# Optimization experiments

Hardware: AMD Instinct MI355X
Metric: run time of the kernel (lower is better)

## Reference

```python
import jax, jax.numpy as jnp
import numpy as np
from jax import lax

H, W = 128, 128
K_JUNC = 300
STEPS = 32
THRESH = 0.008
BIAS_SPAN = 1
SCALE = 5.0
SENTINEL = K_JUNC * K_JUNC


def decode_hafm(angs, dist, bias):
    # angs [B,3,H,W], dist [B,1,H,W], bias [B,1,H,W] -> lines [B,3,H,W,4]
    bias_range = jnp.arange(-BIAS_SPAN, BIAS_SPAN + 1, dtype=jnp.float32).reshape(1, -1, 1, 1)
    d = jnp.clip(dist + bias * bias_range, 0.0, 1.0)  # [B,3,H,W]
    angle0 = (angs[:, 0:1] - 0.5) * jnp.pi * 2
    angle1 = angs[:, 1:2] * jnp.pi / 2
    angle2 = -angs[:, 2:3] * jnp.pi / 2
    c0, s0 = jnp.cos(angle0), jnp.sin(angle0)
    t1, t2 = jnp.tan(angle1), jnp.tan(angle2)
    x1 = (c0 - s0 * t1) * d * SCALE
    y1 = (s0 + c0 * t1) * d * SCALE
    x2 = (c0 - s0 * t2) * d * SCALE
    y2 = (s0 + c0 * t2) * d * SCALE
    y0, x0 = jnp.meshgrid(jnp.arange(H, dtype=jnp.float32), jnp.arange(W, dtype=jnp.float32), indexing='ij')
    x0 = x0[None, None]
    y0 = y0[None, None]
    x1 = jnp.clip(x1 + x0, 0, W - 1)
    y1 = jnp.clip(y1 + y0, 0, H - 1)
    x2 = jnp.clip(x2 + x0, 0, W - 1)
    y2 = jnp.clip(y2 + y0, 0, H - 1)
    return jnp.stack((x1, y1, x2, y2), axis=-1)


def propose_junctions(jloc, joff):
    # jloc [H,W], joff [2,H,W]; 3x3 NMS + top-K, thresholded junctions
    pooled = lax.reduce_window(jloc, -jnp.inf, lax.max, (3, 3), (1, 1), 'SAME')
    nms = jnp.where(jloc == pooled, jloc, 0.0)
    scores, idx = lax.top_k(nms.reshape(-1), K_JUNC)
    y = (idx // W).astype(jnp.float32)
    x = (idx % W).astype(jnp.float32)
    xs = x + joff[0].reshape(-1)[idx]
    ys = y + joff[1].reshape(-1)[idx]
    coords = jnp.stack([xs, ys], axis=-1)  # [K,2]
    valid = scores > THRESH
    coords = jnp.where(valid[:, None], coords, 1e6)
    return coords, scores


def bilinear_sample(fmap, px, py):
    # fmap [C,H,W]; px,py [N,S] -> [C,N,S]
    C = fmap.shape[0]
    px = jnp.clip(px, 0.0, W - 1)
    py = jnp.clip(py, 0.0, H - 1)
    x0 = jnp.floor(px)
    y0 = jnp.floor(py)
    x0i = x0.astype(jnp.int32)
    y0i = y0.astype(jnp.int32)
    x1i = jnp.minimum(x0i + 1, W - 1)
    y1i = jnp.minimum(y0i + 1, H - 1)
    wx = px - x0
    wy = py - y0
    flat = fmap.reshape(C, H * W)

    def g(yi, xi):
        return flat[:, (yi * W + xi).reshape(-1)].reshape(C, *px.shape)

    return (g(y0i, x0i) * (1 - wx) * (1 - wy)
            + g(y0i, x1i) * wx * (1 - wy)
            + g(y1i, x0i) * (1 - wx) * wy
            + g(y1i, x1i) * wx * wy)


def setup_inputs() -> dict:
    key = jax.random.key(0)
    ks = jax.random.split(key, 10)
    return {
        'features': jax.random.normal(ks[0], (1, 256, H, W), jnp.float32),
        'heatmaps': jax.random.normal(ks[1], (1, 9, H, W), jnp.float32),
        'fc1_w': jax.random.normal(ks[2], (128, 256), jnp.float32) * 0.05,
        'fc1_b': jax.random.normal(ks[3], (128,), jnp.float32) * 0.05,
        'w1': jax.random.normal(ks[4], (1024, 1024), jnp.float32) * 0.03,
        'b1': jnp.zeros((1024,), jnp.float32),
        'w2': jax.random.normal(ks[5], (1024, 1024), jnp.float32) * 0.03,
        'b2': jnp.zeros((1024,), jnp.float32),
        'w3': jax.random.normal(ks[6], (1, 1024), jnp.float32) * 0.03,
        'b3': jnp.zeros((1,), jnp.float32),
    }


def reference(features, heatmaps, fc1_w, fc1_b, w1, b1, w2, b2, w3, b3):
    angs = jax.nn.sigmoid(heatmaps[:, 0:3])
    dist = jax.nn.sigmoid(heatmaps[:, 3:4])
    bias = jax.nn.sigmoid(heatmaps[:, 4:5])
    jloc = jax.nn.softmax(heatmaps[:, 5:7], axis=1)[0, 1]  # [H,W]
    joff = jax.nn.sigmoid(heatmaps[0, 7:9])                # [2,H,W]

    junc, _ = propose_junctions(jloc, joff)                # [K,2]
    lines = decode_hafm(angs, dist, bias).reshape(-1, 4)   # [N,4], N=3*H*W
    N = lines.shape[0]

    # junction-to-endpoint matching (cdist + argmin)
    d1 = ((junc[:, None, :] - lines[None, :, :2]) ** 2).sum(-1)  # [K,N]
    d2 = ((junc[:, None, :] - lines[None, :, 2:]) ** 2).sum(-1)
    j1 = jnp.argmin(d1, axis=0)
    j2 = jnp.argmin(d2, axis=0)
    lo = jnp.minimum(j1, j2)
    hi = jnp.maximum(j1, j2)
    ids = jnp.where(lo < hi, lo * K_JUNC + hi, SENTINEL)
    # fixed-size dedup (masked analogue of torch unique(dim=0))
    uids = jnp.unique(ids, size=N, fill_value=SENTINEL)
    valid = uids < SENTINEL
    uids_safe = jnp.where(valid, uids, 0)
    p1 = junc[uids_safe // K_JUNC]
    p2 = junc[uids_safe % K_JUNC]
    line_coords = jnp.where(valid[:, None], jnp.concatenate([p1, p2], axis=-1), 0.0)  # [N,4]

    # LOI feature sampling
    loi = jnp.einsum('oc,chw->ohw', fc1_w, features[0]) + fc1_b[:, None, None]  # [128,H,W]
    t = jnp.linspace(0.0, 1.0, STEPS)[None, :]
    px = line_coords[:, 0:1] * t + line_coords[:, 2:3] * (1 - t)  # [N,32]
    py = line_coords[:, 1:2] * t + line_coords[:, 3:4] * (1 - t)
    feats = bilinear_sample(loi, px, py)            # [128,N,32]
    feats = feats.transpose(1, 0, 2)                # [N,128,32]
    feats = feats.reshape(N, 128, STEPS // 4, 4).max(-1)  # max_pool1d k=4
    feats = feats.reshape(N, 1024)

    h = jax.nn.relu(feats @ w1.T + b1)
    h = jax.nn.relu(h @ w2.T + b2)
    logits = (h @ w3.T + b3)[:, 0]
    line_scores = jax.nn.sigmoid(logits) * valid
    return line_coords, line_scores
```

## Files before the change

### kernel.cpp

```cpp
#include <hip/hip_runtime.h>
#include <math.h>

#define HH 128
#define WW 128
#define HW 16384
#define NLINES 49152
#define KJ 300
#define SENT 90000
#define THRESHV 0.008f
#define CAND_CAP 4096
#define BITWORDS 2816

typedef __attribute__((ext_vector_type(8))) short bf16x8;
typedef __attribute__((ext_vector_type(4))) float f32x4;

__device__ __forceinline__ float sigm(float x){ return 1.0f/(1.0f+expf(-x)); }

__device__ __forceinline__ short tobf(float f){
  unsigned u = __float_as_uint(f);
  unsigned r = u + 0x7FFFu + ((u >> 16) & 1u);
  return (short)(r >> 16);
}
__device__ __forceinline__ float bflo(unsigned u){ return __uint_as_float(u << 16); }
__device__ __forceinline__ float bfhi(unsigned u){ return __uint_as_float(u & 0xFFFF0000u); }

#define GLOAD_LDS16(g, l) \
  __builtin_amdgcn_global_load_lds((const __attribute__((address_space(1))) void*)(g), \
                                   (__attribute__((address_space(3))) void*)(l), 16, 0, 0)

__device__ __forceinline__ float jloc_at(const float* hm, int idx){
  float h5 = hm[5*HW + idx], h6 = hm[6*HW + idx];
  float mx = fmaxf(h5,h6);
  float e5 = expf(h5-mx), e6 = expf(h6-mx);
  return e6/(e5+e6);
}

__global__ __launch_bounds__(256) void k_front(const float* __restrict__ hm,
    const float* __restrict__ feat, const float* __restrict__ fc1w,
    float* __restrict__ lines, unsigned long long* __restrict__ cand,
    int* __restrict__ cand_count, short* __restrict__ featT, short* __restrict__ fc1b16){
  __shared__ float tile[32][33];
  __shared__ float jl[4][128];
  int b = blockIdx.x, t = threadIdx.x;
  if (b < 64){
    int i = b*256 + t;
    float h0 = hm[i], h1 = hm[HW+i], h2 = hm[2*HW+i], h3 = hm[3*HW+i], h4 = hm[4*HW+i];
    float a0 = sigm(h0), a1 = sigm(h1), a2 = sigm(h2);
    float dist = sigm(h3), bias = sigm(h4);
    const float PI = 3.14159265358979323846f;
    float ang0 = (a0-0.5f)*(2.0f*PI);
    float c0 = cosf(ang0), s0 = sinf(ang0);
    float t1 = tanf(a1*(0.5f*PI));
    float t2 = tanf(-a2*(0.5f*PI));
    int y = i >> 7, x = i & 127;
    float fx = (float)x, fy = (float)y;
    #pragma unroll
    for (int c=0;c<3;c++){
      float d = fminf(fmaxf(dist + bias*(float)(c-1), 0.0f), 1.0f);
      float ds = d*5.0f;
      float x1 = fminf(fmaxf((c0 - s0*t1)*ds + fx, 0.0f), 127.0f);
      float y1 = fminf(fmaxf((s0 + c0*t1)*ds + fy, 0.0f), 127.0f);
      float x2 = fminf(fmaxf((c0 - s0*t2)*ds + fx, 0.0f), 127.0f);
      float y2 = fminf(fmaxf((s0 + c0*t2)*ds + fy, 0.0f), 127.0f);
      ((float4*)lines)[c*HW + i] = make_float4(x1,y1,x2,y2);
    }
    int y0 = 2*b;
    #pragma unroll
    for (int idx = t; idx < 512; idx += 256){
      int r = idx >> 7, xx = idx & 127;
      int yy = y0 - 1 + r;
      jl[r][xx] = (yy >= 0 && yy < HH) ? jloc_at(hm, yy*WW + xx) : -1e30f;
    }
    __syncthreads();
    int lr = 1 + (t >> 7);
    float v = jl[lr][x];
    float m = v;
    #pragma unroll
    for (int dy=-1; dy<=1; dy++){
      #pragma unroll
      for (int dx=-1; dx<=1; dx++){
        int nx = x + dx; if (nx < 0 || nx >= WW) continue;
        m = fmaxf(m, jl[lr+dy][nx]);
      }
    }
    if (v == m && v > THRESHV){
      int pos = atomicAdd(cand_count, 1);
      if (pos < CAND_CAP){
        unsigned int vb = __float_as_uint(v);
        cand[pos] = ((unsigned long long)vb << 32) | (unsigned long long)(0xFFFFFFFFu - (unsigned)i);
      }
    }
  } else if (b < 64 + 4096){
    int idx = b - 64;
    int p0 = (idx & 511) * 32, c0 = (idx >> 9) * 32;
    int c  = t >> 3;
    int p4 = (t & 7) * 4;
    float4 v = *(const float4*)&feat[(size_t)(c0 + c)*HW + p0 + p4];
    tile[c][p4+0] = v.x; tile[c][p4+1] = v.y; tile[c][p4+2] = v.z; tile[c][p4+3] = v.w;
    __syncthreads();
    int p  = t >> 3;
    int cg = (t & 7) * 4;
    ushort4 o;
    o.x = (unsigned short)tobf(tile[cg+0][p]);
    o.y = (unsigned short)tobf(tile[cg+1][p]);
    o.z = (unsigned short)tobf(tile[cg+2][p]);
    o.w = (unsigned short)tobf(tile[cg+3][p]);
    *(ushort4*)&featT[(size_t)(p0 + p)*256 + c0 + cg] = o;
  } else {
    int j = (b - 4160)*256 + t;
    fc1b16[j] = tobf(fc1w[j]);
  }
}

__global__ __launch_bounds__(1024) void k_mid(
    const unsigned long long* __restrict__ cand, const int* __restrict__ cand_count,
    const float* __restrict__ hm, float* __restrict__ junc,
    const short* __restrict__ featT, const short* __restrict__ fc1b16,
    const float* __restrict__ fc1b, short* __restrict__ loi){
  __shared__ __align__(16) char smem[CAND_CAP*8];
  int b = blockIdx.x, t = threadIdx.x;
  if (b == 0){
    unsigned long long* s = (unsigned long long*)smem;
    int count = *cand_count; if (count > CAND_CAP) count = CAND_CAP;
    int n2 = 512;
    while (n2 < count) n2 <<= 1;
    for (int i=t; i<n2; i+=1024) s[i] = (i < count) ? cand[i] : 0ull;
    __syncthreads();
    for (int k=2; k<=n2; k<<=1){
      for (int j=k>>1; j>0; j>>=1){
        for (int i=t; i<n2; i+=1024){
          int ixj = i ^ j;
          if (ixj > i){
            unsigned long long a = s[i], bb = s[ixj];
            bool desc = ((i & k) == 0);
            if (desc ? (a < bb) : (a > bb)){ s[i] = bb; s[ixj] = a; }
          }
        }
        __syncthreads();
      }
    }
    if (t < KJ){
      float jx = 1e6f, jy = 1e6f;
      if (t < count){
        unsigned idx = 0xFFFFFFFFu - (unsigned)(s[t] & 0xFFFFFFFFull);
        int yy = (int)(idx >> 7), xx = (int)(idx & 127u);
        jx = (float)xx + sigm(hm[7*HW + idx]);
        jy = (float)yy + sigm(hm[8*HW + idx]);
      }
      junc[2*t] = jx; junc[2*t+1] = jy;
    }
  } else {
    if (t >= 256) return;
    short* As = (short*)smem;
    short* Bs = (short*)(smem + 8192);
    int rb = (b - 1) * 64;
    int lane = t & 63, wave = t >> 6;
    int l16 = lane & 15, quad = lane >> 4;
    int srow = lane >> 3, schunk = (lane & 7) ^ srow;
    f32x4 acc[8];
    #pragma unroll
    for (int g=0; g<8; g++) acc[g] = (f32x4){0,0,0,0};
    for (int k0=0; k0<256; k0+=64){
      #pragma unroll
      for (int i=0; i<2; i++){
        int r0 = wave*16 + i*8;
        GLOAD_LDS16(featT + (size_t)(rb + r0 + srow)*256 + k0 + schunk*8, &As[r0*64]);
      }
      #pragma unroll
      for (int i=0; i<4; i++){
        int r0 = wave*32 + i*8;
        GLOAD_LDS16(fc1b16 + (size_t)(r0 + srow)*256 + k0 + schunk*8, &Bs[r0*64]);
      }
      __syncthreads();
      #pragma unroll
      for (int s2=0; s2<2; s2++){
        int slot = (s2*4 + quad) ^ (l16 & 7);
        bf16x8 a = *(const bf16x8*)&As[(wave*16 + l16)*64 + slot*8];
        #pragma unroll
        for (int g=0; g<8; g++){
          bf16x8 bv = *(const bf16x8*)&Bs[(g*16 + l16)*64 + slot*8];
          acc[g] = __builtin_amdgcn_mfma_f32_16x16x32_bf16(a, bv, acc[g], 0, 0, 0);
        }
      }
      __syncthreads();
    }
    int rowbase = rb + wave*16 + quad*4;
    #pragma unroll
    for (int g=0; g<8; g++){
      int col = g*16 + l16;
      float bs = fc1b[col];
      #pragma unroll
      for (int r=0; r<4; r++)
        loi[(size_t)(rowbase + r)*128 + col] = tobf(acc[g][r] + bs);
    }
  }
}

__global__ __launch_bounds__(256) void k_match(const float* __restrict__ lines,
    const float* __restrict__ junc, unsigned* __restrict__ bm,
    const float* __restrict__ w1, const float* __restrict__ w2,
    short* __restrict__ w1b, short* __restrict__ w2b){
  __shared__ float jx[KJ], jy[KJ];
  int b = blockIdx.x, t = threadIdx.x;
  if (b < 192){
    for (int k=t; k<KJ; k+=256){ jx[k] = junc[2*k]; jy[k] = junc[2*k+1]; }
    __syncthreads();
    int n = b*256 + t;
    float4 L = ((const float4*)lines)[n];
    float b1 = 1e30f, b2 = 1e30f; int j1 = 0, j2 = 0;
    #pragma unroll 4
    for (int k=0; k<KJ; k++){
      float dx1 = jx[k]-L.x, dy1 = jy[k]-L.y;
      float d1 = dx1*dx1 + dy1*dy1;
      float dx2 = jx[k]-L.z, dy2 = jy[k]-L.w;
      float d2 = dx2*dx2 + dy2*dy2;
      if (d1 < b1){ b1 = d1; j1 = k; }
      if (d2 < b2){ b2 = d2; j2 = k; }
    }
    int lo = min(j1,j2), hi = max(j1,j2);
    if (lo < hi){
      int id = lo*KJ + hi;
      atomicOr(&bm[id >> 5], 1u << (id & 31));
    }
  } else {
    int j = (b - 192)*256 + t;
    w1b[j] = tobf(w1[j]);
    w2b[j] = tobf(w2[j]);
  }
}

__global__ __launch_bounds__(1024) void k_unique(const unsigned* __restrict__ bm,
    int* __restrict__ uid_list, int* __restrict__ mcount){
  __shared__ int wsum[16];
  int t = threadIdx.x;
  int w0 = t*3;
  unsigned wv[3];
  int local = 0;
  #pragma unroll
  for (int i=0; i<3; i++){
    int w = w0 + i;
    wv[i] = (w < BITWORDS) ? bm[w] : 0u;
    local += __popc(wv[i]);
  }
  int v = local;
  #pragma unroll
  for (int d=1; d<64; d<<=1){
    int nv = __shfl_up(v, d, 64);
    if ((t & 63) >= d) v += nv;
  }
  if ((t & 63) == 63) wsum[t >> 6] = v;
  __syncthreads();
  if (t < 16){
    int x = wsum[t];
    #pragma unroll
    for (int d=1; d<16; d<<=1){
      int nv = __shfl_up(x, d, 16);
      if (t >= d) x += nv;
    }
    wsum[t] = x;
  }
  __syncthreads();
  int base = v - local + ((t >> 6) ? wsum[(t >> 6) - 1] : 0);
  #pragma unroll
  for (int i=0; i<3; i++){
    unsigned bits = wv[i];
    while (bits){
      int bb = __ffs(bits) - 1;
      uid_list[base++] = (w0 + i)*32 + bb;
      bits &= bits - 1;
    }
  }
  if (t == 1023) *mcount = wsum[15];
}

__global__ __launch_bounds__(256) void k_sample(float* __restrict__ out,
    const int* __restrict__ uid_list, const float* __restrict__ junc,
    const short* __restrict__ loi, const int* __restrict__ mcount,
    short* __restrict__ fbuf, float* __restrict__ logit, int* __restrict__ cnt,
    int ncnt, int chunk0, int chunk){
  __shared__ int4   sOffs[32];
  __shared__ float4 sWts[32];
  int M = *mcount;
  int t = threadIdx.x;
  if (t == 0 && blockIdx.x < ncnt) cnt[blockIdx.x] = 0;
  int q  = t >> 6;
  int c2 = (t & 63) << 1;
  int lim = M - chunk0; if (lim > chunk) lim = chunk;
  for (int l = blockIdx.x; l < lim; l += gridDim.x){
    int r = chunk0 + l;
    if (t == 0) logit[l] = 0.0f;
    __syncthreads();
    if (t < 32){
      int id = uid_list[r];
      int lo = id / KJ, hi = id % KJ;
      float2 P1 = ((const float2*)junc)[lo];
      float2 P2 = ((const float2*)junc)[hi];
      if (t == 0) ((float4*)out)[r] = make_float4(P1.x, P1.y, P2.x, P2.y);
      float tt = (float)t * (1.0f/31.0f);
      float px = P1.x*tt + P2.x*(1.0f-tt);
      float py = P1.y*tt + P2.y*(1.0f-tt);
      px = fminf(fmaxf(px, 0.0f), 127.0f);
      py = fminf(fmaxf(py, 0.0f), 127.0f);
      float x0 = floorf(px), y0 = floorf(py);
      int x0i = (int)x0, y0i = (int)y0;
      int x1i = min(x0i+1, 127), y1i = min(y0i+1, 127);
      float wx = px - x0, wy = py - y0;
      sOffs[t] = make_int4((y0i*WW + x0i)*128, (y0i*WW + x1i)*128,
                           (y1i*WW + x0i)*128, (y1i*WW + x1i)*128);
      sWts[t]  = make_float4((1.0f-wx)*(1.0f-wy), wx*(1.0f-wy),
                             (1.0f-wx)*wy,        wx*wy);
    }
    __syncthreads();
    float gl0=-1e30f, gl1=-1e30f, gh0=-1e30f, gh1=-1e30f;
    #pragma unroll
    for (int j=0; j<8; j++){
      int s = q*8 + j;
      int4 o   = sOffs[s];
      float4 w = sWts[s];
      unsigned u00 = *(const unsigned*)&loi[o.x + c2];
      unsigned u01 = *(const unsigned*)&loi[o.y + c2];
      unsigned u10 = *(const unsigned*)&loi[o.z + c2];
      unsigned u11 = *(const unsigned*)&loi[o.w + c2];
      float vlo = w.x*bflo(u00) + w.y*bflo(u01) + w.z*bflo(u10) + w.w*bflo(u11);
      float vhi = w.x*bfhi(u00) + w.y*bfhi(u01) + w.z*bfhi(u10) + w.w*bfhi(u11);
      if (j < 4){ gl0 = fmaxf(gl0, vlo); gh0 = fmaxf(gh0, vhi); }
      else      { gl1 = fmaxf(gl1, vlo); gh1 = fmaxf(gh1, vhi); }
    }
    unsigned plo = ((unsigned)(unsigned short)tobf(gl0)) | (((unsigned)(unsigned short)tobf(gl1)) << 16);
    unsigned phi = ((unsigned)(unsigned short)tobf(gh0)) | (((unsigned)(unsigned short)tobf(gh1)) << 16);
    *(unsigned*)&fbuf[(size_t)l*1024 + c2*8 + q*2]     = plo;
    *(unsigned*)&fbuf[(size_t)l*1024 + (c2+1)*8 + q*2] = phi;
  }
}

template<int MODE>
__global__ __launch_bounds__(256) void k_mlp(const short* __restrict__ A,
    const short* __restrict__ B, const float* __restrict__ bias,
    short* __restrict__ Hout, const float* __restrict__ w3,
    const float* __restrict__ b3, float* __restrict__ logit,
    int* __restrict__ cnt, const int* __restrict__ mcount,
    int chunk0, float* __restrict__ outScore){
  int M = *mcount;
  int rb = blockIdx.x * 64;
  if (chunk0 + rb >= M) return;
  int cb = blockIdx.y * 128;
  __shared__ short As[64*64];
  __shared__ short Bs[128*64];
  __shared__ int sflag;
  int lane = threadIdx.x & 63, wave = threadIdx.x >> 6;
  int l16 = lane & 15, quad = lane >> 4;
  int srow = lane >> 3, schunk = (lane & 7) ^ srow;
  f32x4 acc[8];
  #pragma unroll
  for (int g=0; g<8; g++) acc[g] = (f32x4){0,0,0,0};
  for (int k0=0; k0<1024; k0+=64){
    #pragma unroll
    for (int i=0; i<2; i++){
      int r0 = wave*16 + i*8;
      GLOAD_LDS16(A + (size_t)(rb + r0 + srow)*1024 + k0 + schunk*8, &As[r0*64]);
    }
    #pragma unroll
    for (int i=0; i<4; i++){
      int r0 = wave*32 + i*8;
      GLOAD_LDS16(B + (size_t)(cb + r0 + srow)*1024 + k0 + schunk*8, &Bs[r0*64]);
    }
    __syncthreads();
    #pragma unroll
    for (int s=0; s<2; s++){
      int slot = (s*4 + quad) ^ (l16 & 7);
      bf16x8 a = *(const bf16x8*)&As[(wave*16 + l16)*64 + slot*8];
      #pragma unroll
      for (int g=0; g<8; g++){
        bf16x8 bv = *(const bf16x8*)&Bs[(g*16 + l16)*64 + slot*8];
        acc[g] = __builtin_amdgcn_mfma_f32_16x16x32_bf16(a, bv, acc[g], 0, 0, 0);
      }
    }
    __syncthreads();
  }
  int rowbase = rb + wave*16 + quad*4;
  if (MODE == 0){
    #pragma unroll
    for (int g=0; g<8; g++){
      int col = cb + g*16 + l16;
      float bs = bias[col];
      #pragma unroll
      for (int r=0; r<4; r++)
        Hout[(size_t)(rowbase + r)*1024 + col] = tobf(fmaxf(acc[g][r] + bs, 0.0f));
    }
  } else {
    float p0[4] = {0,0,0,0};
    #pragma unroll
    for (int g=0; g<8; g++){
      int col = cb + g*16 + l16;
      float bs = bias[col], wv = w3[col];
      #pragma unroll
      for (int r=0; r<4; r++)
        p0[r] += fmaxf(acc[g][r] + bs, 0.0f) * wv;
    }
    #pragma unroll
    for (int r=0; r<4; r++){
      #pragma unroll
      for (int m=1; m<16; m<<=1)
        p0[r] += __shfl_xor(p0[r], m, 16);
    }
    if (l16 == 0){
      #pragma unroll
      for (int r=0; r<4; r++)
        atomicAdd(&logit[rowbase + r], p0[r]);
    }
    __syncthreads();
    if (threadIdx.x == 0){
      __threadfence();
      int old = atomicAdd(&cnt[blockIdx.x], 1);
      sflag = (old == 7) ? 1 : 0;
    }
    __syncthreads();
    if (sflag){
      __threadfence();
      if (threadIdx.x < 64){
        int row = rb + threadIdx.x;
        int rg = chunk0 + row;
        if (rg < M){
          float lg = atomicAdd(&logit[row], 0.0f) + b3[0];
          outScore[4*NLINES + rg] = 1.0f/(1.0f + expf(-lg));
        }
      }
    }
  }
}

extern "C" void kernel_launch(void* const* d_in, const int* in_sizes, int n_in,
                              void* d_out, int out_size, void* d_ws, size_t ws_size,
                              hipStream_t stream){
  const float* features = (const float*)d_in[0];
  const float* heatmaps = (const float*)d_in[1];
  const float* fc1_w    = (const float*)d_in[2];
  const float* fc1_b    = (const float*)d_in[3];
  const float* w1       = (const float*)d_in[4];
  const float* b1       = (const float*)d_in[5];
  const float* w2       = (const float*)d_in[6];
  const float* b2       = (const float*)d_in[7];
  const float* w3       = (const float*)d_in[8];
  const float* b3       = (const float*)d_in[9];
  float* out = (float*)d_out;

  char* ws = (char*)d_ws;
  size_t off = 0;
  auto alloc = [&](size_t bytes) -> void* {
    void* p = ws + off;
    off = (off + bytes + 255) & ~(size_t)255;
    return p;
  };
  float* lines     = (float*)alloc((size_t)NLINES*16);
  unsigned long long* cand = (unsigned long long*)alloc(CAND_CAP*8);
  int*      cand_count = (int*)alloc(4);
  unsigned* bitmap     = (unsigned*)alloc(BITWORDS*4);
  size_t zlen = (size_t)((char*)(bitmap + BITWORDS) - (char*)cand_count);
  float* junc      = (float*)alloc(KJ*2*4);
  int*   uid_list  = (int*)alloc((size_t)45056*4);
  int*   mcount    = (int*)alloc(4);
  int*   cnt       = (int*)alloc((45056/64)*4);
  short* loi       = (short*)alloc((size_t)HW*128*2);
  short* featT     = (short*)alloc((size_t)HW*256*2);
  short* fc1b16    = (short*)alloc((size_t)128*256*2);
  short* w1b       = (short*)alloc((size_t)1024*1024*2);
  short* w2b       = (short*)alloc((size_t)1024*1024*2);
  size_t fixed = off;

  const int chunk_opts[4] = {45056, 22528, 11264, 5632};
  int CHUNK = 5632;
  for (int ci=0; ci<4; ci++){
    size_t need = fixed + (size_t)chunk_opts[ci]*1024*2*2 + (size_t)chunk_opts[ci]*4 + 1024;
    if (need <= ws_size){ CHUNK = chunk_opts[ci]; break; }
  }
  short* fbuf  = (short*)alloc((size_t)CHUNK*1024*2);
  short* h1buf = (short*)alloc((size_t)CHUNK*1024*2);
  float* logit = (float*)alloc((size_t)CHUNK*4);

  hipMemsetAsync(cand_count, 0, zlen, stream);
  hipMemsetAsync(d_out, 0, (size_t)out_size*4, stream);
  k_front<<<4288, 256, 0, stream>>>(heatmaps, features, fc1_w, lines, cand,
                                    cand_count, featT, fc1b16);
  k_mid  <<<257, 1024, 0, stream>>>(cand, cand_count, heatmaps, junc, featT,
                                    fc1b16, fc1_b, loi);
  k_match<<<4288, 256, 0, stream>>>(lines, junc, bitmap, w1, w2, w1b, w2b);
  k_unique<<<1, 1024, 0, stream>>>(bitmap, uid_list, mcount);

  int nchunk = (45056 + CHUNK - 1) / CHUNK;
  for (int ci=0; ci<nchunk; ci++){
    int chunk0 = ci * CHUNK;
    k_sample<<<2048, 256, 0, stream>>>(out, uid_list, junc, loi, mcount, fbuf,
                                       logit, cnt, CHUNK/64, chunk0, CHUNK);
    dim3 g1(CHUNK/64, 8);
    k_mlp<0><<<g1, 256, 0, stream>>>(fbuf, w1b, b1, h1buf, nullptr, nullptr,
                                     nullptr, nullptr, mcount, chunk0, nullptr);
    k_mlp<2><<<g1, 256, 0, stream>>>(h1buf, w2b, b2, nullptr, w3, b3,
                                     logit, cnt, mcount, chunk0, out);
  }
}
```

Measured before the change: 210.4 us.

## Fuse unique into match via last-block pattern, zero output in front kernel

Removes the separate k_unique launch: the last block of k_match, detected by an atomic counter, scans the bitmap and writes the compacted uid list. The output memset moves into extra blocks of k_front. k_sample now handles two lines per block iteration, sharing one barrier pair, and launches half as many blocks. The goal is fewer launches and barriers, at the cost of a serialized tail in the last match block and the tile-transpose pattern staying the same.

```diff
diff --git a/kernel.cpp b/kernel.cpp
--- a/kernel.cpp
+++ b/kernel.cpp
@@ -38,7 +38,8 @@
 __global__ __launch_bounds__(256) void k_front(const float* __restrict__ hm,
     const float* __restrict__ feat, const float* __restrict__ fc1w,
     float* __restrict__ lines, unsigned long long* __restrict__ cand,
-    int* __restrict__ cand_count, short* __restrict__ featT, short* __restrict__ fc1b16){
+    int* __restrict__ cand_count, short* __restrict__ featT, short* __restrict__ fc1b16,
+    float* __restrict__ outZero){
   __shared__ float tile[32][33];
   __shared__ float jl[4][128];
   int b = blockIdx.x, t = threadIdx.x;
@@ -106,9 +107,12 @@
     o.z = (unsigned short)tobf(tile[cg+2][p]);
     o.w = (unsigned short)tobf(tile[cg+3][p]);
     *(ushort4*)&featT[(size_t)(p0 + p)*256 + c0 + cg] = o;
-  } else {
+  } else if (b < 4288){
     int j = (b - 4160)*256 + t;
     fc1b16[j] = tobf(fc1w[j]);
+  } else {
+    int j = (b - 4288)*256 + t;
+    ((float4*)outZero)[j] = make_float4(0.f,0.f,0.f,0.f);
   }
 }
 
@@ -198,9 +202,12 @@
 
 __global__ __launch_bounds__(256) void k_match(const float* __restrict__ lines,
     const float* __restrict__ junc, unsigned* __restrict__ bm,
+    int* __restrict__ mdone, int* __restrict__ uid_list, int* __restrict__ mcount,
     const float* __restrict__ w1, const float* __restrict__ w2,
     short* __restrict__ w1b, short* __restrict__ w2b){
   __shared__ float jx[KJ], jy[KJ];
+  __shared__ int wsum[4];
+  __shared__ int lastflag;
   int b = blockIdx.x, t = threadIdx.x;
   if (b < 192){
     for (int k=t; k<KJ; k+=256){ jx[k] = junc[2*k]; jy[k] = junc[2*k+1]; }
@@ -227,20 +234,20 @@
     w1b[j] = tobf(w1[j]);
     w2b[j] = tobf(w2[j]);
   }
-}
-
-__global__ __launch_bounds__(1024) void k_unique(const unsigned* __restrict__ bm,
-    int* __restrict__ uid_list, int* __restrict__ mcount){
-  __shared__ int wsum[16];
-  int t = threadIdx.x;
-  int w0 = t*3;
-  unsigned wv[3];
+  __syncthreads();
+  if (t == 0){
+    __threadfence();
+    int old = atomicAdd(mdone, 1);
+    lastflag = (old == (int)gridDim.x - 1) ? 1 : 0;
+  }
+  __syncthreads();
+  if (!lastflag) return;
+  unsigned w[11];
   int local = 0;
   #pragma unroll
-  for (int i=0; i<3; i++){
-    int w = w0 + i;
-    wv[i] = (w < BITWORDS) ? bm[w] : 0u;
-    local += __popc(wv[i]);
+  for (int i=0; i<11; i++){
+    w[i] = atomicOr(&bm[t*11 + i], 0u);
+    local += __popc(w[i]);
   }
   int v = local;
   #pragma unroll
@@ -250,11 +257,11 @@
   }
   if ((t & 63) == 63) wsum[t >> 6] = v;
   __syncthreads();
-  if (t < 16){
+  if (t < 4){
     int x = wsum[t];
     #pragma unroll
-    for (int d=1; d<16; d<<=1){
-      int nv = __shfl_up(x, d, 16);
+    for (int d=1; d<4; d<<=1){
+      int nv = __shfl_up(x, d, 4);
       if (t >= d) x += nv;
     }
     wsum[t] = x;
@@ -262,15 +269,15 @@
   __syncthreads();
   int base = v - local + ((t >> 6) ? wsum[(t >> 6) - 1] : 0);
   #pragma unroll
-  for (int i=0; i<3; i++){
-    unsigned bits = wv[i];
+  for (int i=0; i<11; i++){
+    unsigned bits = w[i];
     while (bits){
       int bb = __ffs(bits) - 1;
-      uid_list[base++] = (w0 + i)*32 + bb;
+      uid_list[base++] = (t*11 + i)*32 + bb;
       bits &= bits - 1;
     }
   }
-  if (t == 1023) *mcount = wsum[15];
+  if (t == 255) *mcount = wsum[3];
 }
 
 __global__ __launch_bounds__(256) void k_sample(float* __restrict__ out,
@@ -278,58 +285,69 @@
     const short* __restrict__ loi, const int* __restrict__ mcount,
     short* __restrict__ fbuf, float* __restrict__ logit, int* __restrict__ cnt,
     int ncnt, int chunk0, int chunk){
-  __shared__ int4   sOffs[32];
-  __shared__ float4 sWts[32];
+  __shared__ int4   sOffs[2][32];
+  __shared__ float4 sWts[2][32];
   int M = *mcount;
   int t = threadIdx.x;
   if (t == 0 && blockIdx.x < ncnt) cnt[blockIdx.x] = 0;
   int q  = t >> 6;
   int c2 = (t & 63) << 1;
   int lim = M - chunk0; if (lim > chunk) lim = chunk;
-  for (int l = blockIdx.x; l < lim; l += gridDim.x){
-    int r = chunk0 + l;
-    if (t == 0) logit[l] = 0.0f;
-    __syncthreads();
-    if (t < 32){
-      int id = uid_list[r];
-      int lo = id / KJ, hi = id % KJ;
-      float2 P1 = ((const float2*)junc)[lo];
-      float2 P2 = ((const float2*)junc)[hi];
-      if (t == 0) ((float4*)out)[r] = make_float4(P1.x, P1.y, P2.x, P2.y);
-      float tt = (float)t * (1.0f/31.0f);
-      float px = P1.x*tt + P2.x*(1.0f-tt);
-      float py = P1.y*tt + P2.y*(1.0f-tt);
-      px = fminf(fmaxf(px, 0.0f), 127.0f);
-      py = fminf(fmaxf(py, 0.0f), 127.0f);
-      float x0 = floorf(px), y0 = floorf(py);
-      int x0i = (int)x0, y0i = (int)y0;
-      int x1i = min(x0i+1, 127), y1i = min(y0i+1, 127);
-      float wx = px - x0, wy = py - y0;
-      sOffs[t] = make_int4((y0i*WW + x0i)*128, (y0i*WW + x1i)*128,
-                           (y1i*WW + x0i)*128, (y1i*WW + x1i)*128);
-      sWts[t]  = make_float4((1.0f-wx)*(1.0f-wy), wx*(1.0f-wy),
-                             (1.0f-wx)*wy,        wx*wy);
-    }
-    __syncthreads();
-    float gl0=-1e30f, gl1=-1e30f, gh0=-1e30f, gh1=-1e30f;
-    #pragma unroll
-    for (int j=0; j<8; j++){
-      int s = q*8 + j;
-      int4 o   = sOffs[s];
-      float4 w = sWts[s];
-      unsigned u00 = *(const unsigned*)&loi[o.x + c2];
-      unsigned u01 = *(const unsigned*)&loi[o.y + c2];
-      unsigned u10 = *(const unsigned*)&loi[o.z + c2];
-      unsigned u11 = *(const unsigned*)&loi[o.w + c2];
-      float vlo = w.x*bflo(u00) + w.y*bflo(u01) + w.z*bflo(u10) + w.w*bflo(u11);
-      float vhi = w.x*bfhi(u00) + w.y*bfhi(u01) + w.z*bfhi(u10) + w.w*bfhi(u11);
-      if (j < 4){ gl0 = fmaxf(gl0, vlo); gh0 = fmaxf(gh0, vhi); }
-      else      { gl1 = fmaxf(gl1, vlo); gh1 = fmaxf(gh1, vhi); }
-    }
-    unsigned plo = ((unsigned)(unsigned short)tobf(gl0)) | (((unsigned)(unsigned short)tobf(gl1)) << 16);
-    unsigned phi = ((unsigned)(unsigned short)tobf(gh0)) | (((unsigned)(unsigned short)tobf(gh1)) << 16);
-    *(unsigned*)&fbuf[(size_t)l*1024 + c2*8 + q*2]     = plo;
-    *(unsigned*)&fbuf[(size_t)l*1024 + (c2+1)*8 + q*2] = phi;
+  for (int l0 = blockIdx.x*2; l0 < lim; l0 += gridDim.x*2){
+    __syncthreads();
+    if (t < 64){
+      int pair = t >> 5, s = t & 31;
+      int l = l0 + pair;
+      if (l < lim){
+        int r = chunk0 + l;
+        int id = uid_list[r];
+        int lo = id / KJ, hi = id % KJ;
+        float2 P1 = ((const float2*)junc)[lo];
+        float2 P2 = ((const float2*)junc)[hi];
+        if (s == 0){
+          ((float4*)out)[r] = make_float4(P1.x, P1.y, P2.x, P2.y);
+          logit[l] = 0.0f;
+        }
+        float tt = (float)s * (1.0f/31.0f);
+        float px = P1.x*tt + P2.x*(1.0f-tt);
+        float py = P1.y*tt + P2.y*(1.0f-tt);
+        px = fminf(fmaxf(px, 0.0f), 127.0f);
+        py = fminf(fmaxf(py, 0.0f), 127.0f);
+        float x0 = floorf(px), y0 = floorf(py);
+        int x0i = (int)x0, y0i = (int)y0;
+        int x1i = min(x0i+1, 127), y1i = min(y0i+1, 127);
+        float wx = px - x0, wy = py - y0;
+        sOffs[pair][s] = make_int4((y0i*WW + x0i)*128, (y0i*WW + x1i)*128,
+                                   (y1i*WW + x0i)*128, (y1i*WW + x1i)*128);
+        sWts[pair][s]  = make_float4((1.0f-wx)*(1.0f-wy), wx*(1.0f-wy),
+                                     (1.0f-wx)*wy,        wx*wy);
+      }
+    }
+    __syncthreads();
+    #pragma unroll
+    for (int pair=0; pair<2; pair++){
+      int l = l0 + pair;
+      if (l >= lim) break;
+      float gl0=-1e30f, gl1=-1e30f, gh0=-1e30f, gh1=-1e30f;
+      #pragma unroll
+      for (int j=0; j<8; j++){
+        int s = q*8 + j;
+        int4 o   = sOffs[pair][s];
+        float4 w = sWts[pair][s];
+        unsigned u00 = *(const unsigned*)&loi[o.x + c2];
+        unsigned u01 = *(const unsigned*)&loi[o.y + c2];
+        unsigned u10 = *(const unsigned*)&loi[o.z + c2];
+        unsigned u11 = *(const unsigned*)&loi[o.w + c2];
+        float vlo = w.x*bflo(u00) + w.y*bflo(u01) + w.z*bflo(u10) + w.w*bflo(u11);
+        float vhi = w.x*bfhi(u00) + w.y*bfhi(u01) + w.z*bfhi(u10) + w.w*bfhi(u11);
+        if (j < 4){ gl0 = fmaxf(gl0, vlo); gh0 = fmaxf(gh0, vhi); }
+        else      { gl1 = fmaxf(gl1, vlo); gh1 = fmaxf(gh1, vhi); }
+      }
+      unsigned plo = ((unsigned)(unsigned short)tobf(gl0)) | (((unsigned)(unsigned short)tobf(gl1)) << 16);
+      unsigned phi = ((unsigned)(unsigned short)tobf(gh0)) | (((unsigned)(unsigned short)tobf(gh1)) << 16);
+      *(unsigned*)&fbuf[(size_t)l*1024 + c2*8 + q*2]     = plo;
+      *(unsigned*)&fbuf[(size_t)l*1024 + (c2+1)*8 + q*2] = phi;
+    }
   }
 }
 
@@ -454,6 +472,7 @@
   float* lines     = (float*)alloc((size_t)NLINES*16);
   unsigned long long* cand = (unsigned long long*)alloc(CAND_CAP*8);
   int*      cand_count = (int*)alloc(4);
+  int*      mdone      = (int*)alloc(4);
   unsigned* bitmap     = (unsigned*)alloc(BITWORDS*4);
   size_t zlen = (size_t)((char*)(bitmap + BITWORDS) - (char*)cand_count);
   float* junc      = (float*)alloc(KJ*2*4);
@@ -478,18 +497,17 @@
   float* logit = (float*)alloc((size_t)CHUNK*4);
 
   hipMemsetAsync(cand_count, 0, zlen, stream);
-  hipMemsetAsync(d_out, 0, (size_t)out_size*4, stream);
-  k_front<<<4288, 256, 0, stream>>>(heatmaps, features, fc1_w, lines, cand,
-                                    cand_count, featT, fc1b16);
+  k_front<<<4528, 256, 0, stream>>>(heatmaps, features, fc1_w, lines, cand,
+                                    cand_count, featT, fc1b16, out);
   k_mid  <<<257, 1024, 0, stream>>>(cand, cand_count, heatmaps, junc, featT,
                                     fc1b16, fc1_b, loi);
-  k_match<<<4288, 256, 0, stream>>>(lines, junc, bitmap, w1, w2, w1b, w2b);
-  k_unique<<<1, 1024, 0, stream>>>(bitmap, uid_list, mcount);
+  k_match<<<4288, 256, 0, stream>>>(lines, junc, bitmap, mdone, uid_list, mcount,
+                                    w1, w2, w1b, w2b);
 
   int nchunk = (45056 + CHUNK - 1) / CHUNK;
   for (int ci=0; ci<nchunk; ci++){
     int chunk0 = ci * CHUNK;
-    k_sample<<<2048, 256, 0, stream>>>(out, uid_list, junc, loi, mcount, fbuf,
+    k_sample<<<1024, 256, 0, stream>>>(out, uid_list, junc, loi, mcount, fbuf,
                                        logit, cnt, CHUNK/64, chunk0, CHUNK);
     dim3 g1(CHUNK/64, 8);
     k_mlp<0><<<g1, 256, 0, stream>>>(fbuf, w1b, b1, h1buf, nullptr, nullptr,
```

Measured after the change: 290.5 us. 1.38x slower.

## Replace atomic completion counter with separate score kernel; fold output zeroing into k_front

Applied to the files above, without the earlier changes.

Removes the per-block atomic counter and threadfence-based last-block detection in the second MLP kernel and moves the sigmoid scoring into a small separate k_score kernel. The hipMemset of the output is replaced by extra blocks in k_front that zero it with float4 stores. k_sample now processes two lines per block iteration, halving the grid and the number of barriers per line. The trade is an extra kernel launch per chunk in exchange for less fence and atomic serialization.

```diff
diff --git a/kernel.cpp b/kernel.cpp
--- a/kernel.cpp
+++ b/kernel.cpp
@@ -38,7 +38,8 @@
 __global__ __launch_bounds__(256) void k_front(const float* __restrict__ hm,
     const float* __restrict__ feat, const float* __restrict__ fc1w,
     float* __restrict__ lines, unsigned long long* __restrict__ cand,
-    int* __restrict__ cand_count, short* __restrict__ featT, short* __restrict__ fc1b16){
+    int* __restrict__ cand_count, short* __restrict__ featT, short* __restrict__ fc1b16,
+    float* __restrict__ outZero){
   __shared__ float tile[32][33];
   __shared__ float jl[4][128];
   int b = blockIdx.x, t = threadIdx.x;
@@ -106,9 +107,12 @@
     o.z = (unsigned short)tobf(tile[cg+2][p]);
     o.w = (unsigned short)tobf(tile[cg+3][p]);
     *(ushort4*)&featT[(size_t)(p0 + p)*256 + c0 + cg] = o;
-  } else {
+  } else if (b < 4288){
     int j = (b - 4160)*256 + t;
     fc1b16[j] = tobf(fc1w[j]);
+  } else {
+    int j = (b - 4288)*256 + t;
+    ((float4*)outZero)[j] = make_float4(0.f,0.f,0.f,0.f);
   }
 }
 
@@ -276,60 +280,69 @@
 __global__ __launch_bounds__(256) void k_sample(float* __restrict__ out,
     const int* __restrict__ uid_list, const float* __restrict__ junc,
     const short* __restrict__ loi, const int* __restrict__ mcount,
-    short* __restrict__ fbuf, float* __restrict__ logit, int* __restrict__ cnt,
-    int ncnt, int chunk0, int chunk){
-  __shared__ int4   sOffs[32];
-  __shared__ float4 sWts[32];
+    short* __restrict__ fbuf, float* __restrict__ logit, int chunk0, int chunk){
+  __shared__ int4   sOffs[2][32];
+  __shared__ float4 sWts[2][32];
   int M = *mcount;
   int t = threadIdx.x;
-  if (t == 0 && blockIdx.x < ncnt) cnt[blockIdx.x] = 0;
   int q  = t >> 6;
   int c2 = (t & 63) << 1;
   int lim = M - chunk0; if (lim > chunk) lim = chunk;
-  for (int l = blockIdx.x; l < lim; l += gridDim.x){
-    int r = chunk0 + l;
-    if (t == 0) logit[l] = 0.0f;
-    __syncthreads();
-    if (t < 32){
-      int id = uid_list[r];
-      int lo = id / KJ, hi = id % KJ;
-      float2 P1 = ((const float2*)junc)[lo];
-      float2 P2 = ((const float2*)junc)[hi];
-      if (t == 0) ((float4*)out)[r] = make_float4(P1.x, P1.y, P2.x, P2.y);
-      float tt = (float)t * (1.0f/31.0f);
-      float px = P1.x*tt + P2.x*(1.0f-tt);
-      float py = P1.y*tt + P2.y*(1.0f-tt);
-      px = fminf(fmaxf(px, 0.0f), 127.0f);
-      py = fminf(fmaxf(py, 0.0f), 127.0f);
-      float x0 = floorf(px), y0 = floorf(py);
-      int x0i = (int)x0, y0i = (int)y0;
-      int x1i = min(x0i+1, 127), y1i = min(y0i+1, 127);
-      float wx = px - x0, wy = py - y0;
-      sOffs[t] = make_int4((y0i*WW + x0i)*128, (y0i*WW + x1i)*128,
-                           (y1i*WW + x0i)*128, (y1i*WW + x1i)*128);
-      sWts[t]  = make_float4((1.0f-wx)*(1.0f-wy), wx*(1.0f-wy),
-                             (1.0f-wx)*wy,        wx*wy);
-    }
-    __syncthreads();
-    float gl0=-1e30f, gl1=-1e30f, gh0=-1e30f, gh1=-1e30f;
-    #pragma unroll
-    for (int j=0; j<8; j++){
-      int s = q*8 + j;
-      int4 o   = sOffs[s];
-      float4 w = sWts[s];
-      unsigned u00 = *(const unsigned*)&loi[o.x + c2];
-      unsigned u01 = *(const unsigned*)&loi[o.y + c2];
-      unsigned u10 = *(const unsigned*)&loi[o.z + c2];
-      unsigned u11 = *(const unsigned*)&loi[o.w + c2];
-      float vlo = w.x*bflo(u00) + w.y*bflo(u01) + w.z*bflo(u10) + w.w*bflo(u11);
-      float vhi = w.x*bfhi(u00) + w.y*bfhi(u01) + w.z*bfhi(u10) + w.w*bfhi(u11);
-      if (j < 4){ gl0 = fmaxf(gl0, vlo); gh0 = fmaxf(gh0, vhi); }
-      else      { gl1 = fmaxf(gl1, vlo); gh1 = fmaxf(gh1, vhi); }
-    }
-    unsigned plo = ((unsigned)(unsigned short)tobf(gl0)) | (((unsigned)(unsigned short)tobf(gl1)) << 16);
-    unsigned phi = ((unsigned)(unsigned short)tobf(gh0)) | (((unsigned)(unsigned short)tobf(gh1)) << 16);
-    *(unsigned*)&fbuf[(size_t)l*1024 + c2*8 + q*2]     = plo;
-    *(unsigned*)&fbuf[(size_t)l*1024 + (c2+1)*8 + q*2] = phi;
+  for (int l0 = blockIdx.x*2; l0 < lim; l0 += gridDim.x*2){
+    __syncthreads();
+    if (t < 64){
+      int pair = t >> 5, s = t & 31;
+      int l = l0 + pair;
+      if (l < lim){
+        int r = chunk0 + l;
+        int id = uid_list[r];
+        int lo = id / KJ, hi = id % KJ;
+        float2 P1 = ((const float2*)junc)[lo];
+        float2 P2 = ((const float2*)junc)[hi];
+        if (s == 0){
+          ((float4*)out)[r] = make_float4(P1.x, P1.y, P2.x, P2.y);
+          logit[l] = 0.0f;
+        }
+        float tt = (float)s * (1.0f/31.0f);
+        float px = P1.x*tt + P2.x*(1.0f-tt);
+        float py = P1.y*tt + P2.y*(1.0f-tt);
+        px = fminf(fmaxf(px, 0.0f), 127.0f);
+        py = fminf(fmaxf(py, 0.0f), 127.0f);
+        float x0 = floorf(px), y0 = floorf(py);
+        int x0i = (int)x0, y0i = (int)y0;
+        int x1i = min(x0i+1, 127), y1i = min(y0i+1, 127);
+        float wx = px - x0, wy = py - y0;
+        sOffs[pair][s] = make_int4((y0i*WW + x0i)*128, (y0i*WW + x1i)*128,
+                                   (y1i*WW + x0i)*128, (y1i*WW + x1i)*128);
+        sWts[pair][s]  = make_float4((1.0f-wx)*(1.0f-wy), wx*(1.0f-wy),
+                                     (1.0f-wx)*wy,        wx*wy);
+      }
+    }
+    __syncthreads();
+    #pragma unroll
+    for (int pair=0; pair<2; pair++){
+      int l = l0 + pair;
+      if (l >= lim) break;
+      float gl0=-1e30f, gl1=-1e30f, gh0=-1e30f, gh1=-1e30f;
+      #pragma unroll
+      for (int j=0; j<8; j++){
+        int s = q*8 + j;
+        int4 o   = sOffs[pair][s];
+        float4 w = sWts[pair][s];
+        unsigned u00 = *(const unsigned*)&loi[o.x + c2];
+        unsigned u01 = *(const unsigned*)&loi[o.y + c2];
+        unsigned u10 = *(const unsigned*)&loi[o.z + c2];
+        unsigned u11 = *(const unsigned*)&loi[o.w + c2];
+        float vlo = w.x*bflo(u00) + w.y*bflo(u01) + w.z*bflo(u10) + w.w*bflo(u11);
+        float vhi = w.x*bfhi(u00) + w.y*bfhi(u01) + w.z*bfhi(u10) + w.w*bfhi(u11);
+        if (j < 4){ gl0 = fmaxf(gl0, vlo); gh0 = fmaxf(gh0, vhi); }
+        else      { gl1 = fmaxf(gl1, vlo); gh1 = fmaxf(gh1, vhi); }
+      }
+      unsigned plo = ((unsigned)(unsigned short)tobf(gl0)) | (((unsigned)(unsigned short)tobf(gl1)) << 16);
+      unsigned phi = ((unsigned)(unsigned short)tobf(gh0)) | (((unsigned)(unsigned short)tobf(gh1)) << 16);
+      *(unsigned*)&fbuf[(size_t)l*1024 + c2*8 + q*2]     = plo;
+      *(unsigned*)&fbuf[(size_t)l*1024 + (c2+1)*8 + q*2] = phi;
+    }
   }
 }
 
@@ -337,16 +350,13 @@
 __global__ __launch_bounds__(256) void k_mlp(const short* __restrict__ A,
     const short* __restrict__ B, const float* __restrict__ bias,
     short* __restrict__ Hout, const float* __restrict__ w3,
-    const float* __restrict__ b3, float* __restrict__ logit,
-    int* __restrict__ cnt, const int* __restrict__ mcount,
-    int chunk0, float* __restrict__ outScore){
+    float* __restrict__ logit, const int* __restrict__ mcount, int chunk0){
   int M = *mcount;
   int rb = blockIdx.x * 64;
   if (chunk0 + rb >= M) return;
   int cb = blockIdx.y * 128;
   __shared__ short As[64*64];
   __shared__ short Bs[128*64];
-  __shared__ int sflag;
   int lane = threadIdx.x & 63, wave = threadIdx.x >> 6;
   int l16 = lane & 15, quad = lane >> 4;
   int srow = lane >> 3, schunk = (lane & 7) ^ srow;
@@ -408,25 +418,17 @@
       for (int r=0; r<4; r++)
         atomicAdd(&logit[rowbase + r], p0[r]);
     }
-    __syncthreads();
-    if (threadIdx.x == 0){
-      __threadfence();
-      int old = atomicAdd(&cnt[blockIdx.x], 1);
-      sflag = (old == 7) ? 1 : 0;
-    }
-    __syncthreads();
-    if (sflag){
-      __threadfence();
-      if (threadIdx.x < 64){
-        int row = rb + threadIdx.x;
-        int rg = chunk0 + row;
-        if (rg < M){
-          float lg = atomicAdd(&logit[row], 0.0f) + b3[0];
-          outScore[4*NLINES + rg] = 1.0f/(1.0f + expf(-lg));
-        }
-      }
-    }
-  }
+  }
+}
+
+__global__ void k_score(const float* __restrict__ logit, const float* __restrict__ b3,
+                        const int* __restrict__ mcount, float* __restrict__ out, int chunk0){
+  int i = blockIdx.x*blockDim.x + threadIdx.x;
+  int r = chunk0 + i;
+  int M = *mcount;
+  if (r >= M) return;
+  float lg = logit[i] + b3[0];
+  out[4*NLINES + r] = 1.0f/(1.0f + expf(-lg));
 }
 
 extern "C" void kernel_launch(void* const* d_in, const int* in_sizes, int n_in,
@@ -459,7 +461,6 @@
   float* junc      = (float*)alloc(KJ*2*4);
   int*   uid_list  = (int*)alloc((size_t)45056*4);
   int*   mcount    = (int*)alloc(4);
-  int*   cnt       = (int*)alloc((45056/64)*4);
   short* loi       = (short*)alloc((size_t)HW*128*2);
   short* featT     = (short*)alloc((size_t)HW*256*2);
   short* fc1b16    = (short*)alloc((size_t)128*256*2);
@@ -478,9 +479,8 @@
   float* logit = (float*)alloc((size_t)CHUNK*4);
 
   hipMemsetAsync(cand_count, 0, zlen, stream);
-  hipMemsetAsync(d_out, 0, (size_t)out_size*4, stream);
-  k_front<<<4288, 256, 0, stream>>>(heatmaps, features, fc1_w, lines, cand,
-                                    cand_count, featT, fc1b16);
+  k_front<<<4528, 256, 0, stream>>>(heatmaps, features, fc1_w, lines, cand,
+                                    cand_count, featT, fc1b16, out);
   k_mid  <<<257, 1024, 0, stream>>>(cand, cand_count, heatmaps, junc, featT,
                                     fc1b16, fc1_b, loi);
   k_match<<<4288, 256, 0, stream>>>(lines, junc, bitmap, w1, w2, w1b, w2b);
@@ -489,12 +489,13 @@
   int nchunk = (45056 + CHUNK - 1) / CHUNK;
   for (int ci=0; ci<nchunk; ci++){
     int chunk0 = ci * CHUNK;
-    k_sample<<<2048, 256, 0, stream>>>(out, uid_list, junc, loi, mcount, fbuf,
-                                       logit, cnt, CHUNK/64, chunk0, CHUNK);
+    k_sample<<<1024, 256, 0, stream>>>(out, uid_list, junc, loi, mcount, fbuf,
+                                       logit, chunk0, CHUNK);
     dim3 g1(CHUNK/64, 8);
-    k_mlp<0><<<g1, 256, 0, stream>>>(fbuf, w1b, b1, h1buf, nullptr, nullptr,
-                                     nullptr, nullptr, mcount, chunk0, nullptr);
-    k_mlp<2><<<g1, 256, 0, stream>>>(h1buf, w2b, b2, nullptr, w3, b3,
-                                     logit, cnt, mcount, chunk0, out);
-  }
-}
+    k_mlp<0><<<g1, 256, 0, stream>>>(fbuf, w1b, b1, h1buf, nullptr,
+                                     nullptr, mcount, chunk0);
+    k_mlp<2><<<g1, 256, 0, stream>>>(h1buf, w2b, b2, nullptr, w3,
+                                     logit, mcount, chunk0);
+    k_score<<<(CHUNK+255)/256, 256, 0, stream>>>(logit, b3, mcount, out, chunk0);
+  }
+}
```

After: 199.6 us. 1.05x faster.
